# Performance work log

Hardware: AMD Instinct MI355X
Metric: run time of the kernel (lower is better)

The kernel has to match this reference:

```python
import jax, jax.numpy as jnp
import numpy as np

NUM_HEADS = 16  # config.num_attention_heads


def setup_inputs() -> dict:
    key = jax.random.key(0)
    k0, k1, k2 = jax.random.split(key, 3)
    B, S, D = 2, 2048, 2048
    hd = D // NUM_HEADS  # 128
    hidden_states = jax.random.normal(k0, (B, S, D), dtype=jnp.float32)
    c_attn_w = jax.random.normal(k1, (D + 2 * hd, D), dtype=jnp.float32) * 0.02
    c_attn_b = jnp.zeros((D + 2 * hd,), dtype=jnp.float32)
    c_proj_w = jax.random.normal(k2, (D, D), dtype=jnp.float32) * 0.02
    c_proj_b = jnp.zeros((D,), dtype=jnp.float32)
    return {
        "hidden_states": hidden_states,
        "c_attn_w": c_attn_w,
        "c_attn_b": c_attn_b,
        "c_proj_w": c_proj_w,
        "c_proj_b": c_proj_b,
    }


def reference(hidden_states, c_attn_w, c_attn_b, c_proj_w, c_proj_b):
    B, S, D = hidden_states.shape
    H = NUM_HEADS
    hd = D // H
    scale = hd ** -0.5

    # fused QKV projection: [B,S,D] -> [B,S,D+2*hd]
    qkv = hidden_states @ c_attn_w.T + c_attn_b
    # multi-query split: per-head Q, single shared K and V
    q = qkv[..., :D].reshape(B, S, H, hd)        # [B,S,H,hd]
    k = qkv[..., D:D + hd]                       # [B,S,hd]
    v = qkv[..., D + hd:]                        # [B,S,hd]

    # attention scores (full matrix materialized, like the baddbmm path)
    scores = jnp.einsum('bqhd,bkd->bhqk', q, k) * scale  # [B,H,S,S]
    causal = jnp.tril(jnp.ones((S, S), dtype=bool))
    scores = jnp.where(causal, scores, jnp.finfo(scores.dtype).min)
    attn = jax.nn.softmax(scores, axis=-1)

    # context: shared V broadcast across heads
    ctx = jnp.einsum('bhqk,bkd->bqhd', attn, v).reshape(B, S, D)
    out = ctx @ c_proj_w.T + c_proj_b
    return out
```

## Files before the change

kernel.cpp:

```cpp
#include <hip/hip_runtime.h>
#include <hip/hip_bf16.h>
#include <math.h>

typedef unsigned short u16;
typedef __attribute__((ext_vector_type(8))) __bf16 bf16x8;
typedef __attribute__((ext_vector_type(4))) float f32x4;

__device__ inline u16 f2bf(float f) {
  union { float f; unsigned u; } x; x.f = f;
  unsigned r = x.u + 0x7fffu + ((x.u >> 16) & 1u);
  return (u16)(r >> 16);
}

__device__ inline unsigned cvtpk(float lo, float hi) {
  unsigned r;
  asm("v_cvt_pk_bf16_f32 %0, %1, %2" : "=v"(r) : "v"(lo), "v"(hi));
  return r;
}

__device__ inline float fexp2(float x) {
  float r;
  asm("v_exp_f32 %0, %1" : "=v"(r) : "v"(x));
  return r;
}

__device__ inline void async16(const void* g, void* l) {
  __builtin_amdgcn_global_load_lds(
      (const __attribute__((address_space(1))) void*)g,
      (__attribute__((address_space(3))) void*)l, 16, 0, 0);
}

__global__ __launch_bounds__(256) void cast3_kernel(
    const float* __restrict__ hs, const float* __restrict__ aw,
    const float* __restrict__ pw, u16* __restrict__ hs_o,
    u16* __restrict__ aw_o, u16* __restrict__ pw_o) {
  int blk = blockIdx.x;
  const float* in;
  u16* out;
  int i;
  if (blk < 4096) {
    in = hs; out = hs_o; i = blk * 256 + threadIdx.x;
  } else if (blk < 6400) {
    in = aw; out = aw_o; i = (blk - 4096) * 256 + threadIdx.x;
  } else {
    in = pw; out = pw_o; i = (blk - 6400) * 256 + threadIdx.x;
  }
#pragma unroll
  for (int p = 0; p < 2; ++p) {
    int q = i * 2 + p;
    float4 v = ((const float4*)in)[q];
    u16 o0 = f2bf(v.x), o1 = f2bf(v.y), o2 = f2bf(v.z), o3 = f2bf(v.w);
    unsigned lo = (unsigned)o0 | ((unsigned)o1 << 16);
    unsigned hi = (unsigned)o2 | ((unsigned)o3 << 16);
    ((uint2*)out)[q] = make_uint2(lo, hi);
  }
}

__global__ __launch_bounds__(256) void vt_kernel(
    const u16* __restrict__ qkv, u16* __restrict__ vt) {
  __shared__ u16 tile[32][136];
  const int t = threadIdx.x;
  const int b = blockIdx.x >> 6;
  const int S0 = (blockIdx.x & 63) * 32;
  const int s_l = t >> 3, dg = t & 7;
  const u16* src = qkv + ((size_t)b * 2048 + S0 + s_l) * 2304 + 2176 + dg * 16;
  *(uint4*)&tile[s_l][dg * 16] = *(const uint4*)src;
  *(uint4*)&tile[s_l][dg * 16 + 8] = *(const uint4*)(src + 8);
  __syncthreads();
  const int d = t >> 1, sh = t & 1;
  u16 buf[16];
#pragma unroll
  for (int j = 0; j < 16; ++j) buf[j] = tile[sh * 16 + j][d];
  u16* dst = vt + ((size_t)b * 128 + d) * 2048 + S0 + sh * 16;
  *(uint4*)dst = *(uint4*)&buf[0];
  *(uint4*)(dst + 8) = *(uint4*)&buf[8];
}

template <bool BF16OUT>
__global__ __launch_bounds__(256) void gemm_bt(
    const u16* __restrict__ A, const u16* __restrict__ Bw,
    const float* __restrict__ bias, void* __restrict__ Cout,
    int M, int N, int K, int qcols, float qscale) {
  __shared__ u16 As[2][128 * 64];
  __shared__ u16 Bs[2][128 * 64];
  const int t = threadIdx.x;
  const int w = t >> 6;
  const int lane = t & 63;
  const int lq = lane >> 4, lr = lane & 15;

  int bx = blockIdx.x, by = blockIdx.y;
  const int gx = gridDim.x, gy = gridDim.y;
  if ((gx & 1) == 0 && (gy & 3) == 0) {
    const int cw = gx >> 1, ch = gy >> 2;
    int id = by * gx + bx;
    int xcd = id & 7, j = id >> 3;
    bx = (xcd & 1) * cw + j % cw;
    by = (xcd >> 1) * ch + j / cw;
  }

  const long brow = (long)by * 128;
  const long bcol = (long)bx * 128;
  const int wr = (w >> 1) * 64, wc = (w & 1) * 64;
  f32x4 acc[4][4] = {};

  int rA[4], cA[4];
#pragma unroll
  for (int it = 0; it < 4; ++it) {
    int ci = it * 256 + t;
    rA[it] = ci >> 3;
    cA[it] = (ci & 7) ^ (rA[it] & 7);
  }

  char* const AsB = (char*)&As[0][0];
  char* const BsB = (char*)&Bs[0][0];

  auto stage = [&](int buf, int kt) {
    char* ad = AsB + buf * 16384;
    char* bd = BsB + buf * 16384;
#pragma unroll
    for (int it = 0; it < 4; ++it) {
      const u16* srcA = A + (brow + rA[it]) * (long)K + kt + cA[it] * 8;
      async16(srcA, ad + (it * 256 + w * 64) * 16);
      const u16* srcB = Bw + (bcol + rA[it]) * (long)K + kt + cA[it] * 8;
      async16(srcB, bd + (it * 256 + w * 64) * 16);
    }
  };

  const int swz = ((lr & 4) << 4) + ((lq << 4) ^ ((lr & 3) << 4));
  const int aB0 = (wr + lr) * 128 + swz;
  const int bB0 = (wc + lr) * 128 + swz;
  const char* const a00 = AsB + aB0;
  const char* const a01 = AsB + (aB0 ^ 64);
  const char* const a10 = AsB + 16384 + aB0;
  const char* const a11 = AsB + 16384 + (aB0 ^ 64);
  const char* const b00 = BsB + bB0;
  const char* const b01 = BsB + (bB0 ^ 64);
  const char* const b10 = BsB + 16384 + bB0;
  const char* const b11 = BsB + 16384 + (bB0 ^ 64);

  auto computeK = [&](const char* a0, const char* a1, const char* b0,
                      const char* b1) {
    bf16x8 af[4], bfr[4];
#pragma unroll
    for (int m = 0; m < 4; ++m) af[m] = *(const bf16x8*)(a0 + m * 2048);
#pragma unroll
    for (int n = 0; n < 4; ++n) bfr[n] = *(const bf16x8*)(b0 + n * 2048);
#pragma unroll
    for (int m = 0; m < 4; ++m)
#pragma unroll
      for (int n = 0; n < 4; ++n)
        acc[m][n] = __builtin_amdgcn_mfma_f32_16x16x32_bf16(
            af[m], bfr[n], acc[m][n], 0, 0, 0);
#pragma unroll
    for (int m = 0; m < 4; ++m) af[m] = *(const bf16x8*)(a1 + m * 2048);
#pragma unroll
    for (int n = 0; n < 4; ++n) bfr[n] = *(const bf16x8*)(b1 + n * 2048);
#pragma unroll
    for (int m = 0; m < 4; ++m)
#pragma unroll
      for (int n = 0; n < 4; ++n)
        acc[m][n] = __builtin_amdgcn_mfma_f32_16x16x32_bf16(
            af[m], bfr[n], acc[m][n], 0, 0, 0);
  };

  stage(0, 0);
  __syncthreads();

  for (int kt = 0; kt < K; kt += 128) {
    if (kt + 64 < K) stage(1, kt + 64);
    computeK(a00, a01, b00, b01);
    __syncthreads();
    if (kt + 128 < K) stage(0, kt + 128);
    computeK(a10, a11, b10, b11);
    __syncthreads();
  }

#pragma unroll
  for (int m = 0; m < 4; ++m) {
    long row0 = brow + wr + m * 16 + lq * 4;
#pragma unroll
    for (int n = 0; n < 4; ++n) {
      long col = bcol + wc + n * 16 + lr;
      float bv = bias[col];
      float cs = (col < qcols) ? qscale : 1.f;
#pragma unroll
      for (int j = 0; j < 4; ++j) {
        float v = (acc[m][n][j] + bv) * cs;
        if (BF16OUT)
          ((u16*)Cout)[(row0 + j) * N + col] = f2bf(v);
        else
          ((float*)Cout)[(row0 + j) * N + col] = v;
      }
    }
  }
}

__global__ __launch_bounds__(256, 2) void attn_kernel(
    const u16* __restrict__ qkv, const u16* __restrict__ vt,
    u16* __restrict__ ctx) {
  __shared__ u16 Kl[2][64 * 136];
  __shared__ u16 Vl[2][128 * 72];

  const int t = threadIdx.x;
  const int w = t >> 6;
  const int lane = t & 63;
  const int lq = lane >> 4, lr = lane & 15;
  const int lkey = lq * 4;
  const int kbase8 = lq << 3;
  const int bid = blockIdx.x;
  const int qtid = bid >> 5;
  const int qt = (qtid < 8) ? (15 - qtid) : (qtid - 8);
  const int hb = bid & 31;
  const int h = hb & 15;
  const int b = hb >> 4;
  const int s0w = qt * 128 + w * 32;
  const size_t qb = (size_t)b * 2048 * 2304;

  bf16x8 qg[2][4];
#pragma unroll
  for (int s = 0; s < 2; ++s)
#pragma unroll
    for (int kc = 0; kc < 4; ++kc)
      qg[s][kc] = *(const bf16x8*)(qkv + qb +
                                   (size_t)(s0w + s * 16 + lr) * 2304 +
                                   h * 128 + kc * 32 + lq * 8);

  const u16* kp[5];
  const u16* vp[5];
#pragma unroll
  for (int ii = 0; ii < 5; ++ii) {
    int I = 4 * ii + w;
    {
      int pp = I * 1024 + lane * 16;
      int row = pp / 272;
      int rem = pp - row * 272;
      int ch = (rem < 256) ? (rem >> 4) : 0;
      if (row > 63) row = 63;
      int g = row >> 4, lqr = row & 15;
      int key = ((g & 1) << 5) + ((lqr >> 2) << 3) + ((g >> 1) << 2) +
                (lqr & 3);
      kp[ii] = qkv + qb + (size_t)key * 2304 + 2048 + ch * 8;
    }
    {
      int pp = I * 1024 + lane * 16;
      int row = pp / 144;
      int rem = pp - row * 144;
      int ch = (rem < 128) ? (rem >> 4) : 0;
      if (row > 127) row = 127;
      vp[ii] = vt + ((size_t)b * 128 + row) * 2048 + ch * 8;
    }
  }
  char* const KlB = (char*)&Kl[0][0];
  char* const VlB = (char*)&Vl[0][0];

  auto stage = [&](int buf) {
    char* kd = KlB + buf * 17408;
    char* vd = VlB + buf * 18432;
#pragma unroll
    for (int ii = 0; ii < 5; ++ii) {
      int I = 4 * ii + w;
      if (I < 17) {
        async16(kp[ii], kd + I * 1024);
        kp[ii] += 64 * 2304;
      }
    }
#pragma unroll
    for (int ii = 0; ii < 5; ++ii) {
      int I = 4 * ii + w;
      if (I < 18) {
        async16(vp[ii], vd + I * 1024);
        vp[ii] += 64;
      }
    }
  };

  const int loK = lr * 272 + lq * 16;
  const int loV = lr * 144 + lq * 16;

  float mreg[2] = {-INFINITY, -INFINITY};
  float lreg[2] = {0.f, 0.f};
  f32x4 o[2][8] = {};
  const int ntiles = 2 * qt + 2;

  stage(0);
  __syncthreads();

  int cur = 0;
  for (int j2 = 0; j2 < ntiles; ++j2) {
    const int kvb = j2 * 64;
    if (j2 + 1 < ntiles) stage(cur ^ 1);
    if (kvb <= s0w + 31) {
      const char* KL = KlB + cur * 17408 + loK;
      const char* VL = VlB + cur * 18432 + loV;
      const bool maskT = (kvb + 63 > s0w);

      f32x4 sc[2][4] = {};
#pragma unroll
      for (int g = 0; g < 4; ++g)
#pragma unroll
        for (int kc = 0; kc < 4; ++kc) {
          bf16x8 kf = *(const bf16x8*)(KL + g * 4352 + kc * 64);
          sc[0][g] = __builtin_amdgcn_mfma_f32_16x16x32_bf16(kf, qg[0][kc],
                                                             sc[0][g], 0, 0, 0);
          sc[1][g] = __builtin_amdgcn_mfma_f32_16x16x32_bf16(kf, qg[1][kc],
                                                             sc[1][g], 0, 0, 0);
        }

      bf16x8 vf[16];
#pragma unroll
      for (int n = 0; n < 8; ++n) {
        vf[2 * n] = *(const bf16x8*)(VL + n * 2304);
        vf[2 * n + 1] = *(const bf16x8*)(VL + n * 2304 + 64);
      }

      bf16x8 pa[2][2];
#pragma unroll
      for (int s = 0; s < 2; ++s) {
        float vv[16];
#pragma unroll
        for (int uu = 0; uu < 16; ++uu) vv[uu] = sc[s][uu >> 2][uu & 3];
        if (maskT) {
          const int qrel = s0w + s * 16 + lr - kvb - kbase8;
#pragma unroll
          for (int g = 0; g < 4; ++g)
#pragma unroll
            for (int r = 0; r < 4; ++r)
              if (((g & 1) << 5) + ((g >> 1) << 2) + r > qrel)
                vv[g * 4 + r] = -INFINITY;
        }
        float mx = vv[0];
#pragma unroll
        for (int uu = 1; uu < 16; ++uu) mx = fmaxf(mx, vv[uu]);
        mx = fmaxf(mx, __shfl_xor(mx, 16));
        mx = fmaxf(mx, __shfl_xor(mx, 32));
        float mn = mreg[s];
        if (__any(mx > mn + 8.f)) {
          float mu = fmaxf(mn, mx);
          float alpha = fexp2(mn - mu);
          mreg[s] = mu;
          mn = mu;
          lreg[s] *= alpha;
          float a0 = __shfl(alpha, lkey + 0);
          float a1 = __shfl(alpha, lkey + 1);
          float a2 = __shfl(alpha, lkey + 2);
          float a3 = __shfl(alpha, lkey + 3);
#pragma unroll
          for (int n = 0; n < 8; ++n) {
            o[s][n][0] *= a0;
            o[s][n][1] *= a1;
            o[s][n][2] *= a2;
            o[s][n][3] *= a3;
          }
        }
        float e[16];
        float rs = 0.f;
#pragma unroll
        for (int uu = 0; uu < 16; ++uu) {
          e[uu] = fexp2(vv[uu] - mn);
          rs += e[uu];
        }
        lreg[s] += rs;
        union { unsigned uw[4]; bf16x8 v; } pk;
#pragma unroll
        for (int kc = 0; kc < 2; ++kc) {
          pk.uw[0] = cvtpk(e[kc * 4 + 0], e[kc * 4 + 1]);
          pk.uw[1] = cvtpk(e[kc * 4 + 2], e[kc * 4 + 3]);
          pk.uw[2] = cvtpk(e[(kc + 2) * 4 + 0], e[(kc + 2) * 4 + 1]);
          pk.uw[3] = cvtpk(e[(kc + 2) * 4 + 2], e[(kc + 2) * 4 + 3]);
          pa[s][kc] = pk.v;
        }
      }

#pragma unroll
      for (int n = 0; n < 8; ++n) {
        o[0][n] = __builtin_amdgcn_mfma_f32_16x16x32_bf16(pa[0][0], vf[2 * n],
                                                          o[0][n], 0, 0, 0);
        o[0][n] = __builtin_amdgcn_mfma_f32_16x16x32_bf16(
            pa[0][1], vf[2 * n + 1], o[0][n], 0, 0, 0);
        o[1][n] = __builtin_amdgcn_mfma_f32_16x16x32_bf16(pa[1][0], vf[2 * n],
                                                          o[1][n], 0, 0, 0);
        o[1][n] = __builtin_amdgcn_mfma_f32_16x16x32_bf16(
            pa[1][1], vf[2 * n + 1], o[1][n], 0, 0, 0);
      }
    }
    __syncthreads();
    cur ^= 1;
  }

#pragma unroll
  for (int s = 0; s < 2; ++s) {
    float lsum = lreg[s];
    lsum += __shfl_xor(lsum, 16);
    lsum += __shfl_xor(lsum, 32);
    float inv = 1.f / lsum;
    float iv[4];
    iv[0] = __shfl(inv, lkey + 0);
    iv[1] = __shfl(inv, lkey + 1);
    iv[2] = __shfl(inv, lkey + 2);
    iv[3] = __shfl(inv, lkey + 3);
#pragma unroll
    for (int r = 0; r < 4; ++r) {
      size_t rowoff =
          ((size_t)b * 2048 + s0w + s * 16 + lkey + r) * 2048 + h * 128;
#pragma unroll
      for (int n = 0; n < 8; ++n)
        ctx[rowoff + n * 16 + lr] = f2bf(o[s][n][r] * iv[r]);
    }
  }
}

extern "C" void kernel_launch(void* const* d_in, const int* in_sizes, int n_in,
                              void* d_out, int out_size, void* d_ws,
                              size_t ws_size, hipStream_t stream) {
  (void)in_sizes; (void)n_in; (void)out_size; (void)ws_size;
  const float* hs = (const float*)d_in[0];
  const float* attn_w = (const float*)d_in[1];
  const float* attn_b = (const float*)d_in[2];
  const float* proj_w = (const float*)d_in[3];
  const float* proj_b = (const float*)d_in[4];
  float* out = (float*)d_out;

  u16* hs_b = (u16*)d_ws;
  u16* aw_b = hs_b + (size_t)4096 * 2048;
  u16* pw_b = aw_b + (size_t)2304 * 2048;
  u16* qkv_b = pw_b + (size_t)2048 * 2048;
  u16* vt_b = qkv_b + (size_t)4096 * 2304;
  u16* ctx_b = vt_b + (size_t)2 * 128 * 2048;

  const float qscale = 0.08838834764831845f * 1.4426950408889634f;

  cast3_kernel<<<8448, 256, 0, stream>>>(hs, attn_w, proj_w, hs_b, aw_b,
                                         pw_b);

  gemm_bt<true><<<dim3(18, 32), 256, 0, stream>>>(hs_b, aw_b, attn_b, qkv_b,
                                                  4096, 2304, 2048, 2048,
                                                  qscale);
  vt_kernel<<<128, 256, 0, stream>>>(qkv_b, vt_b);
  attn_kernel<<<512, 256, 0, stream>>>(qkv_b, vt_b, ctx_b);
  gemm_bt<false><<<dim3(16, 32), 256, 0, stream>>>(ctx_b, pw_b, proj_b, out,
                                                   4096, 2048, 2048, 0, 1.f);
}
```

Baseline: 174.5 us.

## Enlarge GEMM tile to 256x128 with 512 threads and triple-buffered async pipeline

The bf16 GEMM now uses 8 waves per block on a 256x128 output tile, so the B tile is shared across twice as many rows. It also switches from a two-stage to a three-stage LDS ring, using explicit vmcnt waits and a single barrier per 64-wide K step. Global source pointers are precomputed and advanced incrementally, which removes per-stage address arithmetic. The cost is more LDS per block (about 144KB), fewer blocks per CU and fewer blocks in the grid (288 and 256), which may leave some CUs idle on a 256-CU part.

```diff
diff --git a/kernel.cpp b/kernel.cpp
--- a/kernel.cpp
+++ b/kernel.cpp
@@ -77,12 +77,12 @@
 }
 
 template <bool BF16OUT>
-__global__ __launch_bounds__(256) void gemm_bt(
+__global__ __launch_bounds__(512) void gemm_bt(
     const u16* __restrict__ A, const u16* __restrict__ Bw,
     const float* __restrict__ bias, void* __restrict__ Cout,
     int M, int N, int K, int qcols, float qscale) {
-  __shared__ u16 As[2][128 * 64];
-  __shared__ u16 Bs[2][128 * 64];
+  __shared__ u16 As[3][256 * 64];
+  __shared__ u16 Bs[3][128 * 64];
   const int t = threadIdx.x;
   const int w = t >> 6;
   const int lane = t & 63;
@@ -98,59 +98,65 @@
     by = (xcd >> 1) * ch + j / cw;
   }
 
-  const long brow = (long)by * 128;
+  const long brow = (long)by * 256;
   const long bcol = (long)bx * 128;
-  const int wr = (w >> 1) * 64, wc = (w & 1) * 64;
+  const int wr = (w >> 1) * 64;
+  const int wc = (w & 1) * 64;
   f32x4 acc[4][4] = {};
 
-  int rA[4], cA[4];
+  const u16* pA[4];
+  const u16* pB[2];
 #pragma unroll
   for (int it = 0; it < 4; ++it) {
-    int ci = it * 256 + t;
-    rA[it] = ci >> 3;
-    cA[it] = (ci & 7) ^ (rA[it] & 7);
-  }
-
-  char* const AsB = (char*)&As[0][0];
-  char* const BsB = (char*)&Bs[0][0];
-
-  auto stage = [&](int buf, int kt) {
-    char* ad = AsB + buf * 16384;
-    char* bd = BsB + buf * 16384;
+    int ci = it * 512 + t;
+    int row = ci >> 3;
+    int ch = (ci & 7) ^ (row & 7);
+    pA[it] = A + (brow + row) * (long)K + ch * 8;
+  }
+#pragma unroll
+  for (int it = 0; it < 2; ++it) {
+    int ci = it * 512 + t;
+    int row = ci >> 3;
+    int ch = (ci & 7) ^ (row & 7);
+    pB[it] = Bw + (bcol + row) * (long)K + ch * 8;
+  }
+
+  char* const A0 = (char*)&As[0][0];
+  char* const B0 = (char*)&Bs[0][0];
+  const int stB = t * 16;
+
+  auto stageTo = [&](char* aAn, char* bAn) {
 #pragma unroll
     for (int it = 0; it < 4; ++it) {
-      const u16* srcA = A + (brow + rA[it]) * (long)K + kt + cA[it] * 8;
-      async16(srcA, ad + (it * 256 + w * 64) * 16);
-      const u16* srcB = Bw + (bcol + rA[it]) * (long)K + kt + cA[it] * 8;
-      async16(srcB, bd + (it * 256 + w * 64) * 16);
+      async16(pA[it], aAn + it * 8192 + stB);
+      pA[it] += 64;
+    }
+#pragma unroll
+    for (int it = 0; it < 2; ++it) {
+      async16(pB[it], bAn + it * 8192 + stB);
+      pB[it] += 64;
     }
   };
 
   const int swz = ((lr & 4) << 4) + ((lq << 4) ^ ((lr & 3) << 4));
-  const int aB0 = (wr + lr) * 128 + swz;
-  const int bB0 = (wc + lr) * 128 + swz;
-  const char* const a00 = AsB + aB0;
-  const char* const a01 = AsB + (aB0 ^ 64);
-  const char* const a10 = AsB + 16384 + aB0;
-  const char* const a11 = AsB + 16384 + (aB0 ^ 64);
-  const char* const b00 = BsB + bB0;
-  const char* const b01 = BsB + (bB0 ^ 64);
-  const char* const b10 = BsB + 16384 + bB0;
-  const char* const b11 = BsB + 16384 + (bB0 ^ 64);
-
-  auto computeK = [&](const char* a0, const char* a1, const char* b0,
-                      const char* b1) {
+  const int aOff = (wr + lr) * 128 + swz;
+  const int bOff = (wc + lr) * 128 + swz;
+  const int dx = (swz ^ 64) - swz;
+
+  auto computeF = [&](const char* aR, const char* bR) {
     bf16x8 af[4], bfr[4];
 #pragma unroll
-    for (int m = 0; m < 4; ++m) af[m] = *(const bf16x8*)(a0 + m * 2048);
-#pragma unroll
-    for (int n = 0; n < 4; ++n) bfr[n] = *(const bf16x8*)(b0 + n * 2048);
+    for (int m = 0; m < 4; ++m) af[m] = *(const bf16x8*)(aR + m * 2048);
+#pragma unroll
+    for (int n = 0; n < 4; ++n) bfr[n] = *(const bf16x8*)(bR + n * 2048);
 #pragma unroll
     for (int m = 0; m < 4; ++m)
 #pragma unroll
       for (int n = 0; n < 4; ++n)
         acc[m][n] = __builtin_amdgcn_mfma_f32_16x16x32_bf16(
             af[m], bfr[n], acc[m][n], 0, 0, 0);
+    const char* a1 = aR + dx;
+    const char* b1 = bR + dx;
 #pragma unroll
     for (int m = 0; m < 4; ++m) af[m] = *(const bf16x8*)(a1 + m * 2048);
 #pragma unroll
@@ -163,16 +169,38 @@
             af[m], bfr[n], acc[m][n], 0, 0, 0);
   };
 
-  stage(0, 0);
-  __syncthreads();
-
-  for (int kt = 0; kt < K; kt += 128) {
-    if (kt + 64 < K) stage(1, kt + 64);
-    computeK(a00, a01, b00, b01);
-    __syncthreads();
-    if (kt + 128 < K) stage(0, kt + 128);
-    computeK(a10, a11, b10, b11);
-    __syncthreads();
+  const char* ar0 = A0 + aOff;
+  const char* ar1 = A0 + 32768 + aOff;
+  const char* ar2 = A0 + 65536 + aOff;
+  const char* br0 = B0 + bOff;
+  const char* br1 = B0 + 16384 + bOff;
+  const char* br2 = B0 + 32768 + bOff;
+  char* sa0 = A0;
+  char* sa1 = A0 + 32768;
+  char* sa2 = A0 + 65536;
+  char* sb0 = B0;
+  char* sb1 = B0 + 16384;
+  char* sb2 = B0 + 32768;
+
+  const int nst = K >> 6;
+  stageTo(sa0, sb0);
+  stageTo(sa1, sb1);
+  asm volatile("s_waitcnt vmcnt(6)" ::: "memory");
+  __builtin_amdgcn_s_barrier();
+
+  for (int s = 0; s < nst; ++s) {
+    const bool st = (s + 2 < nst);
+    if (st) stageTo(sa2, sb2);
+    computeF(ar0, br0);
+    if (st)
+      asm volatile("s_waitcnt vmcnt(6) lgkmcnt(0)" ::: "memory");
+    else
+      asm volatile("s_waitcnt vmcnt(0) lgkmcnt(0)" ::: "memory");
+    __builtin_amdgcn_s_barrier();
+    const char* ta = ar0; ar0 = ar1; ar1 = ar2; ar2 = ta;
+    const char* tb = br0; br0 = br1; br1 = br2; br2 = tb;
+    char* tsa = sa0; sa0 = sa1; sa1 = sa2; sa2 = tsa;
+    char* tsb = sb0; sb0 = sb1; sb1 = sb2; sb2 = tsb;
   }
 
 #pragma unroll
@@ -432,11 +460,11 @@
   cast3_kernel<<<8448, 256, 0, stream>>>(hs, attn_w, proj_w, hs_b, aw_b,
                                          pw_b);
 
-  gemm_bt<true><<<dim3(18, 32), 256, 0, stream>>>(hs_b, aw_b, attn_b, qkv_b,
+  gemm_bt<true><<<dim3(18, 16), 512, 0, stream>>>(hs_b, aw_b, attn_b, qkv_b,
                                                   4096, 2304, 2048, 2048,
                                                   qscale);
   vt_kernel<<<128, 256, 0, stream>>>(qkv_b, vt_b);
   attn_kernel<<<512, 256, 0, stream>>>(qkv_b, vt_b, ctx_b);
-  gemm_bt<false><<<dim3(16, 32), 256, 0, stream>>>(ctx_b, pw_b, proj_b, out,
+  gemm_bt<false><<<dim3(16, 16), 512, 0, stream>>>(ctx_b, pw_b, proj_b, out,
                                                    4096, 2048, 2048, 0, 1.f);
 }
```

Measured after the change: 213.6 us. 22.4% more time.
